# Kernel optimization log

Hardware: AMD Instinct MI355X
Metric: run time of the kernel (lower is better)

## Reference

```python
import jax, jax.numpy as jnp
import numpy as np

N = 100000  # nodes
E = 1600000  # edges
N_IN, N_H = 256, 128


def _norms(edge_src, edge_dst):
    ones = jnp.ones((E,), dtype=jnp.float32)
    out_deg = jax.ops.segment_sum(ones, edge_src, num_segments=N)
    in_deg = jax.ops.segment_sum(ones, edge_dst, num_segments=N)
    # DGL clamps degrees to >= 1 for norm='both'
    norm_src = jnp.clip(out_deg, 1.0, None) ** -0.5  # [N]
    norm_dst = jnp.clip(in_deg, 1.0, None) ** -0.5   # [N]
    return norm_src, norm_dst


def _graph_conv(h, W, b, edge_src, edge_dst, norm_src, norm_dst):
    # symmetric norm: D_out^{-1/2} A D_in^{-1/2}; W applied pre-aggregation
    h = h * norm_src[:, None]          # [N, d_in]
    h = h @ W                          # [N, d_out]
    msg = h[edge_src]                  # [E, d_out] gather
    agg = jax.ops.segment_sum(msg, edge_dst, num_segments=N)  # scatter-add
    agg = agg * norm_dst[:, None]
    return jax.nn.relu(agg + b)


def setup_inputs() -> dict:
    key = jax.random.key(0)
    ks = jax.random.split(key, 7)
    feat = jax.random.normal(ks[0], (1, N, N_IN), dtype=jnp.float32)
    edge_src = jax.random.randint(ks[1], (E,), 0, N, dtype=jnp.int32)
    edge_dst = jax.random.randint(ks[2], (E,), 0, N, dtype=jnp.int32)
    # Glorot-uniform weights as in DGL GraphConv reset_parameters
    lim1 = (6.0 / (N_IN + N_H)) ** 0.5
    lim2 = (6.0 / (N_H + N_H)) ** 0.5
    W1 = jax.random.uniform(ks[3], (N_IN, N_H), jnp.float32, -lim1, lim1)
    b1 = jnp.zeros((N_H,), dtype=jnp.float32)
    W2 = jax.random.uniform(ks[4], (N_H, N_H), jnp.float32, -lim2, lim2)
    b2 = jnp.zeros((N_H,), dtype=jnp.float32)
    return {"feat": feat, "W1": W1, "b1": b1, "W2": W2, "b2": b2,
            "edge_src": edge_src, "edge_dst": edge_dst}


def reference(feat, W1, b1, W2, b2, edge_src, edge_dst):
    h = feat.squeeze(0)  # [N, n_in]
    norm_src, norm_dst = _norms(edge_src, edge_dst)
    h = _graph_conv(h, W1, b1, edge_src, edge_dst, norm_src, norm_dst)
    h = _graph_conv(h, W2, b2, edge_src, edge_dst, norm_src, norm_dst)
    return h
```

## Files before the change

kernel.cpp:

```cpp
#include <hip/hip_runtime.h>
#include <hip/hip_bf16.h>

#define N_NODES 100000
#define N_EDGES 1600000
#define NBUCK 391
#define NBLK 256
#define CHUNK (N_EDGES / NBLK)
#define MATP (NBUCK * NBLK)

typedef float f32x4 __attribute__((ext_vector_type(4)));
typedef unsigned short u16x8 __attribute__((ext_vector_type(8)));
typedef _Float16 f16x8 __attribute__((ext_vector_type(8)));

__device__ __forceinline__ void wt_elem(const float* __restrict__ W,
                                        _Float16* __restrict__ WTf,
                                        int K, int i) {
    int col = i / K, k = i - col * K;
    WTf[i] = (_Float16)W[(size_t)k * 128 + col];
}

__global__ __launch_bounds__(256) void fused_setup(
    const int* __restrict__ esrc, const int* __restrict__ edst,
    int* __restrict__ cnt_mat,
    const float* __restrict__ W1, _Float16* __restrict__ WT1f,
    const float* __restrict__ W2, _Float16* __restrict__ WT2f)
{
    __shared__ int hd[NBUCK], hs[NBUCK];
    const int b = blockIdx.x, t = threadIdx.x;
    if (b < NBLK) {
        for (int i = t; i < NBUCK; i += 256) { hd[i] = 0; hs[i] = 0; }
        __syncthreads();
        const int e1 = (b + 1) * CHUNK;
        for (int e = b * CHUNK + t; e < e1; e += 256) {
            atomicAdd(&hd[edst[e] >> 8], 1);
            atomicAdd(&hs[esrc[e] >> 8], 1);
        }
        __syncthreads();
        for (int i = t; i < NBUCK; i += 256) {
            cnt_mat[i * NBLK + b] = hd[i];
            cnt_mat[MATP + i * NBLK + b] = hs[i];
        }
    } else {
        int i = (b - NBLK) * 256 + t;
        if (i < 128 * 256) {
            wt_elem(W1, WT1f, 256, i);
        } else {
            int j = i - 128 * 256;
            wt_elem(W2, WT2f, 128, j);
        }
    }
}

__global__ __launch_bounds__(1024) void scan_blocks(const int* __restrict__ counts,
                                                    int* __restrict__ out,
                                                    int* __restrict__ partials, int n) {
    __shared__ int tmp[1024];
    int i = blockIdx.x * 1024 + threadIdx.x;
    int v = (i < n) ? counts[i] : 0;
    tmp[threadIdx.x] = v;
    __syncthreads();
    for (int off = 1; off < 1024; off <<= 1) {
        int t = (threadIdx.x >= (unsigned)off) ? tmp[threadIdx.x - off] : 0;
        __syncthreads();
        tmp[threadIdx.x] += t;
        __syncthreads();
    }
    if (i < n) out[i] = tmp[threadIdx.x] - v;
    if (threadIdx.x == 1023) partials[blockIdx.x] = tmp[1023];
}

__global__ __launch_bounds__(256) void scan_partials(int* __restrict__ partials, int nb) {
    __shared__ int tmp[256];
    int t = threadIdx.x;
    int v = (t < nb) ? partials[t] : 0;
    tmp[t] = v;
    __syncthreads();
    for (int off = 1; off < 256; off <<= 1) {
        int u = (t >= off) ? tmp[t - off] : 0;
        __syncthreads();
        tmp[t] += u;
        __syncthreads();
    }
    if (t < nb) partials[t] = tmp[t] - v;
}

__device__ __forceinline__ int sm_at(const int* __restrict__ scan_mat,
                                     const int* __restrict__ partials, int i) {
    return scan_mat[i] + partials[i >> 10];
}

__global__ __launch_bounds__(256) void bucket_scatter(const int* __restrict__ esrc,
                                                      const int* __restrict__ edst,
                                                      const int* __restrict__ scan_mat,
                                                      const int* __restrict__ partials,
                                                      unsigned int* __restrict__ tmp) {
    __shared__ int cd[NBUCK], cs[NBUCK];
    const int b = blockIdx.x, t = threadIdx.x;
    for (int i = t; i < NBUCK; i += 256) {
        cd[i] = sm_at(scan_mat, partials, i * NBLK + b);
        cs[i] = sm_at(scan_mat, partials, MATP + i * NBLK + b);
    }
    __syncthreads();
    const int e1 = (b + 1) * CHUNK;
    for (int e = b * CHUNK + t; e < e1; e += 256) {
        int s = esrc[e], d = edst[e];
        int pd = atomicAdd(&cd[d >> 8], 1);
        tmp[pd] = ((unsigned int)(d & 255) << 17) | (unsigned int)s;
        int ps = atomicAdd(&cs[s >> 8], 1);
        tmp[ps] = (unsigned int)s;
    }
}

__global__ __launch_bounds__(256) void finalize_fused(
    const unsigned int* __restrict__ tmp,
    const int* __restrict__ scan_mat,
    const int* __restrict__ partials,
    int* __restrict__ rowptr,
    int* __restrict__ csr_src,
    float* __restrict__ ndst,
    float* __restrict__ nsrc)
{
    __shared__ int hist[256];
    __shared__ int scn[256];
    __shared__ int cur[256];
    const int bb = blockIdx.x, t = threadIdx.x;
    if (bb < NBUCK) {
        const int b = bb;
        const int beg = sm_at(scan_mat, partials, b * 256);
        const int end = sm_at(scan_mat, partials, (b + 1) * 256);
        hist[t] = 0;
        __syncthreads();
        for (int j = beg + t; j < end; j += 256)
            atomicAdd(&hist[tmp[j] >> 17], 1);
        __syncthreads();
        int v = hist[t];
        scn[t] = v;
        __syncthreads();
        for (int off = 1; off < 256; off <<= 1) {
            int u = (t >= off) ? scn[t - off] : 0;
            __syncthreads();
            scn[t] += u;
            __syncthreads();
        }
        int excl = scn[t] - v;
        int node = b * 256 + t;
        if (node <= N_NODES) rowptr[node] = beg + excl;
        if (node < N_NODES) ndst[node] = rsqrtf(fmaxf((float)v, 1.0f));
        cur[t] = beg + excl;
        __syncthreads();
        for (int j = beg + t; j < end; j += 256) {
            unsigned int x = tmp[j];
            int pos = atomicAdd(&cur[x >> 17], 1);
            csr_src[pos] = (int)(x & 0x1FFFFu);
        }
    } else {
        const int b = bb - NBUCK;
        const int beg = sm_at(scan_mat, partials, MATP + b * 256);
        const int end = (b < NBUCK - 1) ? sm_at(scan_mat, partials, MATP + (b + 1) * 256)
                                        : 2 * N_EDGES;
        hist[t] = 0;
        __syncthreads();
        for (int j = beg + t; j < end; j += 256)
            atomicAdd(&hist[tmp[j] & 255u], 1);
        __syncthreads();
        int node = b * 256 + t;
        if (node < N_NODES) nsrc[node] = rsqrtf(fmaxf((float)hist[t], 1.0f));
    }
}

template<int K, int ATERMS, typename AT>
__global__ __launch_bounds__(256) void gemm_mfma(
    const AT* __restrict__ A,
    const _Float16* __restrict__ WTf,
    const float* __restrict__ rowscale,
    _Float16* __restrict__ C16,
    int M)
{
    constexpr int ASTR = 520;
    constexpr int BSTR = 1032;
    __shared__ _Float16 Ah[4 * ASTR];
    __shared__ _Float16 Al[ATERMS == 2 ? 4 * ASTR : 8];
    __shared__ _Float16 Bf[4 * BSTR];

    const int tid = threadIdx.x;
    const int bm = blockIdx.x * 64;
    const int lane = tid & 63;
    const int wid = tid >> 6;
    const int wm = wid >> 1;
    const int wn = wid & 1;
    const int lr = lane & 15;
    const int lg = lane >> 4;

    const int st_ar = tid >> 2;
    const int st_s8 = tid & 3;
    const int a_row_g = bm + st_ar;

    f32x4 acc[2][4];
    #pragma unroll
    for (int i = 0; i < 2; ++i)
        #pragma unroll
        for (int j = 0; j < 4; ++j)
            acc[i][j] = (f32x4){0.f, 0.f, 0.f, 0.f};

    float avreg[8];
    f16x8 areg16;
    f16x8 bv[2];

    auto load_tile = [&](int k0) {
        if (a_row_g < M) {
            const AT* ap = &A[(size_t)a_row_g * K + k0 + st_s8 * 8];
            if constexpr (sizeof(AT) == 4) {
                float4 v0 = *reinterpret_cast<const float4*>(ap);
                float4 v1 = *reinterpret_cast<const float4*>(ap + 4);
                avreg[0] = v0.x; avreg[1] = v0.y; avreg[2] = v0.z; avreg[3] = v0.w;
                avreg[4] = v1.x; avreg[5] = v1.y; avreg[6] = v1.z; avreg[7] = v1.w;
            } else {
                areg16 = *reinterpret_cast<const f16x8*>(ap);
            }
        } else {
            if constexpr (sizeof(AT) == 4) {
                #pragma unroll
                for (int j = 0; j < 8; ++j) avreg[j] = 0.f;
            } else {
                #pragma unroll
                for (int j = 0; j < 8; ++j) areg16[j] = (_Float16)0.f;
            }
        }
        #pragma unroll
        for (int i = 0; i < 2; ++i) {
            int lin = tid + i * 256;
            int col = lin >> 2;
            int s8  = lin & 3;
            bv[i] = *reinterpret_cast<const f16x8*>(&WTf[(size_t)col * K + k0 + s8 * 8]);
        }
    };

    load_tile(0);

    for (int k0 = 0; k0 < K; k0 += 32) {
        {
            int off = st_s8 * ASTR + st_ar * 8;
            if constexpr (sizeof(AT) == 4) {
                f16x8 vh, vl;
                #pragma unroll
                for (int j = 0; j < 8; ++j) {
                    _Float16 h = (_Float16)avreg[j];
                    vh[j] = h;
                    vl[j] = (_Float16)(avreg[j] - (float)h);
                }
                *reinterpret_cast<f16x8*>(&Ah[off]) = vh;
                if constexpr (ATERMS == 2)
                    *reinterpret_cast<f16x8*>(&Al[off]) = vl;
            } else {
                *reinterpret_cast<f16x8*>(&Ah[off]) = areg16;
            }
            #pragma unroll
            for (int i = 0; i < 2; ++i) {
                int lin = tid + i * 256;
                int col = lin >> 2;
                int s8  = lin & 3;
                *reinterpret_cast<f16x8*>(&Bf[s8 * BSTR + col * 8]) = bv[i];
            }
        }
        __syncthreads();

        if (k0 + 32 < K) load_tile(k0 + 32);

        {
            f16x8 afh[2], afl[2], bf[4];
            #pragma unroll
            for (int mt = 0; mt < 2; ++mt) {
                int row = wm * 32 + mt * 16 + lr;
                int off = lg * ASTR + row * 8;
                afh[mt] = *reinterpret_cast<const f16x8*>(&Ah[off]);
                if constexpr (ATERMS == 2)
                    afl[mt] = *reinterpret_cast<const f16x8*>(&Al[off]);
            }
            #pragma unroll
            for (int nt = 0; nt < 4; ++nt) {
                int col = wn * 64 + nt * 16 + lr;
                bf[nt] = *reinterpret_cast<const f16x8*>(&Bf[lg * BSTR + col * 8]);
            }
            #pragma unroll
            for (int mt = 0; mt < 2; ++mt) {
                #pragma unroll
                for (int nt = 0; nt < 4; ++nt) {
                    acc[mt][nt] = __builtin_amdgcn_mfma_f32_16x16x32_f16(
                        afh[mt], bf[nt], acc[mt][nt], 0, 0, 0);
                    if constexpr (ATERMS == 2)
                        acc[mt][nt] = __builtin_amdgcn_mfma_f32_16x16x32_f16(
                            afl[mt], bf[nt], acc[mt][nt], 0, 0, 0);
                }
            }
        }
        __syncthreads();
    }

    #pragma unroll
    for (int mt = 0; mt < 2; ++mt) {
        #pragma unroll
        for (int r = 0; r < 4; ++r) {
            int row = bm + wm * 32 + mt * 16 + lg * 4 + r;
            if (row < M) {
                float s = rowscale[row];
                #pragma unroll
                for (int nt = 0; nt < 4; ++nt) {
                    int col = wn * 64 + nt * 16 + lr;
                    C16[(size_t)row * 128 + col] = (_Float16)(acc[mt][nt][r] * s);
                }
            }
        }
    }
}

template<typename OT>
__global__ __launch_bounds__(256) void aggregate16(
    const _Float16* __restrict__ h16,
    const int* __restrict__ rowptr,
    const int* __restrict__ csr_src,
    const float* __restrict__ ndst,
    const float* __restrict__ bias,
    OT* __restrict__ out, int N)
{
    int g = blockIdx.x * blockDim.x + threadIdx.x;
    int node = g >> 4;
    if (node >= N) return;
    int c8 = (g & 15) * 8;
    int beg = rowptr[node];
    int end = rowptr[node + 1];
    float acc[8] = {0.f, 0.f, 0.f, 0.f, 0.f, 0.f, 0.f, 0.f};
    int j = beg;
    for (; j + 3 < end; j += 4) {
        int s0 = csr_src[j];
        int s1 = csr_src[j + 1];
        int s2 = csr_src[j + 2];
        int s3 = csr_src[j + 3];
        f16x8 v0 = *reinterpret_cast<const f16x8*>(&h16[(size_t)s0 * 128 + c8]);
        f16x8 v1 = *reinterpret_cast<const f16x8*>(&h16[(size_t)s1 * 128 + c8]);
        f16x8 v2 = *reinterpret_cast<const f16x8*>(&h16[(size_t)s2 * 128 + c8]);
        f16x8 v3 = *reinterpret_cast<const f16x8*>(&h16[(size_t)s3 * 128 + c8]);
        #pragma unroll
        for (int k = 0; k < 8; ++k)
            acc[k] += ((float)v0[k] + (float)v1[k]) + ((float)v2[k] + (float)v3[k]);
    }
    for (; j < end; ++j) {
        int s0 = csr_src[j];
        f16x8 v0 = *reinterpret_cast<const f16x8*>(&h16[(size_t)s0 * 128 + c8]);
        #pragma unroll
        for (int k = 0; k < 8; ++k) acc[k] += (float)v0[k];
    }
    float sc = ndst[node];
    const float4 b0 = *reinterpret_cast<const float4*>(&bias[c8]);
    const float4 b1 = *reinterpret_cast<const float4*>(&bias[c8 + 4]);
    float r[8];
    r[0] = fmaxf(acc[0] * sc + b0.x, 0.f);
    r[1] = fmaxf(acc[1] * sc + b0.y, 0.f);
    r[2] = fmaxf(acc[2] * sc + b0.z, 0.f);
    r[3] = fmaxf(acc[3] * sc + b0.w, 0.f);
    r[4] = fmaxf(acc[4] * sc + b1.x, 0.f);
    r[5] = fmaxf(acc[5] * sc + b1.y, 0.f);
    r[6] = fmaxf(acc[6] * sc + b1.z, 0.f);
    r[7] = fmaxf(acc[7] * sc + b1.w, 0.f);
    OT* op = &out[(size_t)node * 128 + c8];
    if constexpr (sizeof(OT) == 4) {
        float4 r0 = {r[0], r[1], r[2], r[3]};
        float4 r1 = {r[4], r[5], r[6], r[7]};
        *reinterpret_cast<float4*>(op) = r0;
        *reinterpret_cast<float4*>(op + 4) = r1;
    } else {
        f16x8 rv;
        #pragma unroll
        for (int k = 0; k < 8; ++k) rv[k] = (_Float16)r[k];
        *reinterpret_cast<f16x8*>(op) = rv;
    }
}

extern "C" void kernel_launch(void* const* d_in, const int* in_sizes, int n_in,
                              void* d_out, int out_size, void* d_ws, size_t ws_size,
                              hipStream_t stream) {
    const float* feat = (const float*)d_in[0];
    const float* W1   = (const float*)d_in[1];
    const float* b1   = (const float*)d_in[2];
    const float* W2   = (const float*)d_in[3];
    const float* b2   = (const float*)d_in[4];
    const int* esrc   = (const int*)d_in[5];
    const int* edst   = (const int*)d_in[6];
    float* out = (float*)d_out;

    const int Nn = N_NODES, E = N_EDGES;
    const int SCAN_N = 2 * MATP;
    const int SCAN_NB = (SCAN_N + 1023) / 1024;

    float* hseg   = (float*)d_ws;
    _Float16* h16   = (_Float16*)hseg;
    _Float16* h1out = h16 + (size_t)Nn * 128;
    _Float16* WT1f = (_Float16*)(hseg + (size_t)Nn * 128);
    _Float16* WT2f = WT1f + 128 * 256;
    int* csr_src  = (int*)(WT2f + 128 * 128);
    int* rowptr   = csr_src + E;
    unsigned int* tmp = (unsigned int*)(rowptr + 100004);
    int* cnt_mat  = (int*)(tmp + 2 * (size_t)E);
    int* scan_mat = cnt_mat + SCAN_N;
    int* partials = scan_mat + SCAN_N;
    float* nsrc   = (float*)(partials + ((SCAN_NB + 3) & ~3));
    float* ndst   = nsrc + Nn;

    fused_setup<<<NBLK + 192, 256, 0, stream>>>(esrc, edst, cnt_mat, W1, WT1f, W2, WT2f);

    scan_blocks<<<SCAN_NB, 1024, 0, stream>>>(cnt_mat, scan_mat, partials, SCAN_N);
    scan_partials<<<1, 256, 0, stream>>>(partials, SCAN_NB);

    bucket_scatter<<<NBLK, 256, 0, stream>>>(esrc, edst, scan_mat, partials, tmp);
    finalize_fused<<<2 * NBUCK, 256, 0, stream>>>(tmp, scan_mat, partials,
                                                  rowptr, csr_src, ndst, nsrc);

    const int gemm_grid = (Nn + 63) / 64;
    const int agg_grid  = (Nn * 16 + 255) / 256;

    gemm_mfma<256, 2, float><<<gemm_grid, 256, 0, stream>>>(feat, WT1f, nsrc, h16, Nn);
    aggregate16<_Float16><<<agg_grid, 256, 0, stream>>>(
        h16, rowptr, csr_src, ndst, b1, h1out, Nn);

    gemm_mfma<128, 1, _Float16><<<gemm_grid, 256, 0, stream>>>(h1out, WT2f, nsrc, h16, Nn);
    aggregate16<float><<<agg_grid, 256, 0, stream>>>(
        h16, rowptr, csr_src, ndst, b2, out, Nn);
}
```

Before: 225.4 us.

## Store source-degree bucket keys as bytes and double GEMM K-tile depth

The source-side bucket scatter now writes only the low 8 bits of each source id into a separate byte array instead of a full 32-bit word. The out-degree histogram reads that byte array, which cuts scatter write and read traffic for that half of the temp buffer. Separately, the MFMA GEMM now stages 64-wide K tiles instead of 32, halving loop iterations and barriers at the cost of twice the shared memory and more registers per thread. Byte scatters are poorly coalesced, and the larger tile may lower occupancy.

After: 225.3 us. About the same (-0.0%).

```diff
diff --git a/kernel.cpp b/kernel.cpp
--- a/kernel.cpp
+++ b/kernel.cpp
@@ -9,7 +9,6 @@
 #define MATP (NBUCK * NBLK)
 
 typedef float f32x4 __attribute__((ext_vector_type(4)));
-typedef unsigned short u16x8 __attribute__((ext_vector_type(8)));
 typedef _Float16 f16x8 __attribute__((ext_vector_type(8)));
 
 __device__ __forceinline__ void wt_elem(const float* __restrict__ W,
@@ -93,12 +92,13 @@
                                                       const int* __restrict__ edst,
                                                       const int* __restrict__ scan_mat,
                                                       const int* __restrict__ partials,
-                                                      unsigned int* __restrict__ tmp) {
+                                                      unsigned int* __restrict__ tmp,
+                                                      unsigned char* __restrict__ tmp2) {
     __shared__ int cd[NBUCK], cs[NBUCK];
     const int b = blockIdx.x, t = threadIdx.x;
     for (int i = t; i < NBUCK; i += 256) {
         cd[i] = sm_at(scan_mat, partials, i * NBLK + b);
-        cs[i] = sm_at(scan_mat, partials, MATP + i * NBLK + b);
+        cs[i] = sm_at(scan_mat, partials, MATP + i * NBLK + b) - N_EDGES;
     }
     __syncthreads();
     const int e1 = (b + 1) * CHUNK;
@@ -107,12 +107,13 @@
         int pd = atomicAdd(&cd[d >> 8], 1);
         tmp[pd] = ((unsigned int)(d & 255) << 17) | (unsigned int)s;
         int ps = atomicAdd(&cs[s >> 8], 1);
-        tmp[ps] = (unsigned int)s;
+        tmp2[ps] = (unsigned char)(s & 255);
     }
 }
 
 __global__ __launch_bounds__(256) void finalize_fused(
     const unsigned int* __restrict__ tmp,
+    const unsigned char* __restrict__ tmp2,
     const int* __restrict__ scan_mat,
     const int* __restrict__ partials,
     int* __restrict__ rowptr,
@@ -155,13 +156,14 @@
         }
     } else {
         const int b = bb - NBUCK;
-        const int beg = sm_at(scan_mat, partials, MATP + b * 256);
-        const int end = (b < NBUCK - 1) ? sm_at(scan_mat, partials, MATP + (b + 1) * 256)
-                                        : 2 * N_EDGES;
+        const int beg = sm_at(scan_mat, partials, MATP + b * 256) - N_EDGES;
+        const int end = (b < NBUCK - 1)
+                          ? sm_at(scan_mat, partials, MATP + (b + 1) * 256) - N_EDGES
+                          : N_EDGES;
         hist[t] = 0;
         __syncthreads();
         for (int j = beg + t; j < end; j += 256)
-            atomicAdd(&hist[tmp[j] & 255u], 1);
+            atomicAdd(&hist[tmp2[j]], 1);
         __syncthreads();
         int node = b * 256 + t;
         if (node < N_NODES) nsrc[node] = rsqrtf(fmaxf((float)hist[t], 1.0f));
@@ -178,9 +180,9 @@
 {
     constexpr int ASTR = 520;
     constexpr int BSTR = 1032;
-    __shared__ _Float16 Ah[4 * ASTR];
-    __shared__ _Float16 Al[ATERMS == 2 ? 4 * ASTR : 8];
-    __shared__ _Float16 Bf[4 * BSTR];
+    __shared__ _Float16 Ah[8 * ASTR];
+    __shared__ _Float16 Al[ATERMS == 2 ? 8 * ASTR : 8];
+    __shared__ _Float16 Bf[8 * BSTR];
 
     const int tid = threadIdx.x;
     const int bm = blockIdx.x * 64;
@@ -191,10 +193,6 @@
     const int lr = lane & 15;
     const int lg = lane >> 4;
 
-    const int st_ar = tid >> 2;
-    const int st_s8 = tid & 3;
-    const int a_row_g = bm + st_ar;
-
     f32x4 acc[2][4];
     #pragma unroll
     for (int i = 0; i < 2; ++i)
@@ -202,76 +200,91 @@
         for (int j = 0; j < 4; ++j)
             acc[i][j] = (f32x4){0.f, 0.f, 0.f, 0.f};
 
-    float avreg[8];
-    f16x8 areg16;
-    f16x8 bv[2];
+    float avreg[2][8];
+    f16x8 areg16[2];
+    f16x8 bv[4];
 
     auto load_tile = [&](int k0) {
-        if (a_row_g < M) {
-            const AT* ap = &A[(size_t)a_row_g * K + k0 + st_s8 * 8];
-            if constexpr (sizeof(AT) == 4) {
-                float4 v0 = *reinterpret_cast<const float4*>(ap);
-                float4 v1 = *reinterpret_cast<const float4*>(ap + 4);
-                avreg[0] = v0.x; avreg[1] = v0.y; avreg[2] = v0.z; avreg[3] = v0.w;
-                avreg[4] = v1.x; avreg[5] = v1.y; avreg[6] = v1.z; avreg[7] = v1.w;
-            } else {
-                areg16 = *reinterpret_cast<const f16x8*>(ap);
-            }
-        } else {
-            if constexpr (sizeof(AT) == 4) {
-                #pragma unroll
-                for (int j = 0; j < 8; ++j) avreg[j] = 0.f;
-            } else {
-                #pragma unroll
-                for (int j = 0; j < 8; ++j) areg16[j] = (_Float16)0.f;
-            }
-        }
         #pragma unroll
         for (int i = 0; i < 2; ++i) {
             int lin = tid + i * 256;
-            int col = lin >> 2;
-            int s8  = lin & 3;
+            int row = lin >> 3;
+            int s8  = lin & 7;
+            int rg  = bm + row;
+            if (rg < M) {
+                const AT* ap = &A[(size_t)rg * K + k0 + s8 * 8];
+                if constexpr (sizeof(AT) == 4) {
+                    float4 v0 = *reinterpret_cast<const float4*>(ap);
+                    float4 v1 = *reinterpret_cast<const float4*>(ap + 4);
+                    avreg[i][0] = v0.x; avreg[i][1] = v0.y; avreg[i][2] = v0.z; avreg[i][3] = v0.w;
+                    avreg[i][4] = v1.x; avreg[i][5] = v1.y; avreg[i][6] = v1.z; avreg[i][7] = v1.w;
+                } else {
+                    areg16[i] = *reinterpret_cast<const f16x8*>(ap);
+                }
+            } else {
+                if constexpr (sizeof(AT) == 4) {
+                    #pragma unroll
+                    for (int j = 0; j < 8; ++j) avreg[i][j] = 0.f;
+                } else {
+                    #pragma unroll
+                    for (int j = 0; j < 8; ++j) areg16[i][j] = (_Float16)0.f;
+                }
+            }
+        }
+        #pragma unroll
+        for (int i = 0; i < 4; ++i) {
+            int lin = tid + i * 256;
+            int col = lin >> 3;
+            int s8  = lin & 7;
             bv[i] = *reinterpret_cast<const f16x8*>(&WTf[(size_t)col * K + k0 + s8 * 8]);
         }
     };
 
     load_tile(0);
 
-    for (int k0 = 0; k0 < K; k0 += 32) {
+    for (int k0 = 0; k0 < K; k0 += 64) {
         {
-            int off = st_s8 * ASTR + st_ar * 8;
-            if constexpr (sizeof(AT) == 4) {
-                f16x8 vh, vl;
-                #pragma unroll
-                for (int j = 0; j < 8; ++j) {
-                    _Float16 h = (_Float16)avreg[j];
-                    vh[j] = h;
-                    vl[j] = (_Float16)(avreg[j] - (float)h);
-                }
-                *reinterpret_cast<f16x8*>(&Ah[off]) = vh;
-                if constexpr (ATERMS == 2)
-                    *reinterpret_cast<f16x8*>(&Al[off]) = vl;
-            } else {
-                *reinterpret_cast<f16x8*>(&Ah[off]) = areg16;
-            }
             #pragma unroll
             for (int i = 0; i < 2; ++i) {
                 int lin = tid + i * 256;
-                int col = lin >> 2;
-                int s8  = lin & 3;
+                int row = lin >> 3;
+                int s8  = lin & 7;
+                int off = s8 * ASTR + row * 8;
+                if constexpr (sizeof(AT) == 4) {
+                    f16x8 vh, vl;
+                    #pragma unroll
+                    for (int j = 0; j < 8; ++j) {
+                        _Float16 h = (_Float16)avreg[i][j];
+                        vh[j] = h;
+                        vl[j] = (_Float16)(avreg[i][j] - (float)h);
+                    }
+                    *reinterpret_cast<f16x8*>(&Ah[off]) = vh;
+                    if constexpr (ATERMS == 2)
+                        *reinterpret_cast<f16x8*>(&Al[off]) = vl;
+                } else {
+                    *reinterpret_cast<f16x8*>(&Ah[off]) = areg16[i];
+                }
+            }
+            #pragma unroll
+            for (int i = 0; i < 4; ++i) {
+                int lin = tid + i * 256;
+                int col = lin >> 3;
+                int s8  = lin & 7;
                 *reinterpret_cast<f16x8*>(&Bf[s8 * BSTR + col * 8]) = bv[i];
             }
         }
         __syncthreads();
 
-        if (k0 + 32 < K) load_tile(k0 + 32);
-
-        {
+        if (k0 + 64 < K) load_tile(k0 + 64);
+
+        #pragma unroll
+        for (int ks = 0; ks < 2; ++ks) {
+            const int slot = ks * 4 + lg;
             f16x8 afh[2], afl[2], bf[4];
             #pragma unroll
             for (int mt = 0; mt < 2; ++mt) {
                 int row = wm * 32 + mt * 16 + lr;
-                int off = lg * ASTR + row * 8;
+                int off = slot * ASTR + row * 8;
                 afh[mt] = *reinterpret_cast<const f16x8*>(&Ah[off]);
                 if constexpr (ATERMS == 2)
                     afl[mt] = *reinterpret_cast<const f16x8*>(&Al[off]);
@@ -279,7 +292,7 @@
             #pragma unroll
             for (int nt = 0; nt < 4; ++nt) {
                 int col = wn * 64 + nt * 16 + lr;
-                bf[nt] = *reinterpret_cast<const f16x8*>(&Bf[lg * BSTR + col * 8]);
+                bf[nt] = *reinterpret_cast<const f16x8*>(&Bf[slot * BSTR + col * 8]);
             }
             #pragma unroll
             for (int mt = 0; mt < 2; ++mt) {
@@ -399,7 +412,8 @@
     int* csr_src  = (int*)(WT2f + 128 * 128);
     int* rowptr   = csr_src + E;
     unsigned int* tmp = (unsigned int*)(rowptr + 100004);
-    int* cnt_mat  = (int*)(tmp + 2 * (size_t)E);
+    unsigned char* tmp2 = (unsigned char*)(tmp + (size_t)E);
+    int* cnt_mat  = (int*)(tmp2 + (((size_t)E + 15) & ~15ull));
     int* scan_mat = cnt_mat + SCAN_N;
     int* partials = scan_mat + SCAN_N;
     float* nsrc   = (float*)(partials + ((SCAN_NB + 3) & ~3));
@@ -410,8 +424,8 @@
     scan_blocks<<<SCAN_NB, 1024, 0, stream>>>(cnt_mat, scan_mat, partials, SCAN_N);
     scan_partials<<<1, 256, 0, stream>>>(partials, SCAN_NB);
 
-    bucket_scatter<<<NBLK, 256, 0, stream>>>(esrc, edst, scan_mat, partials, tmp);
-    finalize_fused<<<2 * NBUCK, 256, 0, stream>>>(tmp, scan_mat, partials,
+    bucket_scatter<<<NBLK, 256, 0, stream>>>(esrc, edst, scan_mat, partials, tmp, tmp2);
+    finalize_fused<<<2 * NBUCK, 256, 0, stream>>>(tmp, tmp2, scan_mat, partials,
                                                   rowptr, csr_src, ndst, nsrc);
 
     const int gemm_grid = (Nn + 63) / 64;
```
